# Kernel optimization log

Measured on AMD Instinct MI355X. Metric: run time of the kernel, lower is better.

The kernel has to match this reference:

```python
import jax, jax.numpy as jnp
import numpy as np
from jax import lax

B, CIN, COUT, K, H, W = 16, 512, 512, 3, 64, 64
STYLE_DIM, BASIS, DIRS = 512, 8, 8


def setup_inputs() -> dict:
    key = jax.random.key(0)
    ks = jax.random.split(key, 8)
    return {
        "x": jax.random.normal(ks[0], (B, CIN, H, W), jnp.float32),
        "style": jax.random.normal(ks[1], (B, STYLE_DIM), jnp.float32),
        "weight": jax.random.normal(ks[2], (1, COUT, CIN, K, K), jnp.float32),
        "mod_w": jax.random.normal(ks[3], (CIN, STYLE_DIM), jnp.float32) * 0.02,
        "mod_b": jnp.ones((CIN,), jnp.float32),
        "basis_vectors": jax.random.normal(ks[4], (BASIS, 1, COUT, CIN, K, K), jnp.float32),
        "shifts_coords": jax.random.normal(ks[5], (DIRS, BASIS), jnp.float32),
        "batch_shifts": jax.random.uniform(ks[6], (B,), jnp.float32),
        "batch_directions": jax.random.randint(ks[7], (B,), 0, DIRS),
    }


def reference(x, style, weight, mod_w, mod_b, basis_vectors, shifts_coords,
              batch_shifts, batch_directions):
    batch, in_ch, h, w = x.shape
    out_ch, k = weight.shape[1], weight.shape[3]
    scale = 1.0 / np.sqrt(in_ch * k * k)  # StyleGAN2 equalized-lr scale

    # --- deformation: per-sample weight delta from basis subspace ---
    coefs = shifts_coords[batch_directions]                     # [B, basis]
    bv = basis_vectors.reshape(basis_vectors.shape[0], -1)      # [basis, O*I*k*k]
    delta = coefs @ bv                                          # [B, P]
    nrm = jnp.linalg.norm(delta, axis=1, keepdims=True)
    delta = delta / jnp.maximum(nrm, 1e-12) * batch_shifts[:, None]
    delta = delta.reshape(batch, out_ch, in_ch, k, k)
    wgt = weight + delta                                        # [B, O, I, k, k]

    # --- style modulation + demodulation ---
    s = style @ mod_w.T + mod_b                                 # [B, I]
    wgt = scale * wgt * s[:, None, :, None, None]
    demod = lax.rsqrt(jnp.sum(wgt * wgt, axis=(2, 3, 4)) + 1e-8)  # [B, O]
    wgt = wgt * demod[:, :, None, None, None]

    # --- grouped conv, groups = batch ---
    wgt = wgt.reshape(batch * out_ch, in_ch, k, k)
    xg = x.reshape(1, batch * in_ch, h, w)
    pad = k // 2
    out = lax.conv_general_dilated(
        xg, wgt, window_strides=(1, 1), padding=[(pad, pad), (pad, pad)],
        feature_group_count=batch,
        dimension_numbers=("NCHW", "OIHW", "NCHW"))
    return out.reshape(batch, out_ch, h, w)
```

## Files before the change

kernel.cpp:

```cpp
#include <hip/hip_runtime.h>


typedef __attribute__((ext_vector_type(8))) short bf16x8;
typedef __attribute__((ext_vector_type(4))) float f32x4;

__device__ __forceinline__ unsigned short f2bf(float f) {
  unsigned u = __float_as_uint(f);
  return (unsigned short)((u + 0x7FFFu + ((u >> 16) & 1u)) >> 16);
}

__device__ __forceinline__ void gl_lds16(const void* g, void* l) {
  __builtin_amdgcn_global_load_lds(
      (const __attribute__((address_space(1))) void*)g,
      (__attribute__((address_space(3))) void*)l, 16, 0, 0);
}

template <int N> __device__ __forceinline__ void vm_wait() {
  if constexpr (N == 4) asm volatile("s_waitcnt vmcnt(4)" ::: "memory");
  else if constexpr (N == 0) asm volatile("s_waitcnt vmcnt(0)" ::: "memory");
}

__global__ __launch_bounds__(256) void k_pad(const float* __restrict__ x,
                                             unsigned short* __restrict__ xp) {
  const int bx = blockIdx.x;
  const int b   = bx >> 9;
  const int rem = bx & 511;
  const int y   = rem >> 3;
  const int cb  = rem & 7;
  const int t = threadIdx.x;
  __shared__ float tile[64][65];
  const float* src = x + ((size_t)(b * 512 + cb * 64) * 4096) + y * 64;
#pragma unroll
  for (int r = 0; r < 4; ++r) {
    int idx = r * 256 + t;
    int ch = idx >> 4;
    int xq = (idx & 15) << 2;
    float4 v = *(const float4*)(src + (size_t)ch * 4096 + xq);
    tile[ch][xq + 0] = v.x; tile[ch][xq + 1] = v.y;
    tile[ch][xq + 2] = v.z; tile[ch][xq + 3] = v.w;
  }
  const uint4 z4 = {0u, 0u, 0u, 0u};
  if (t < 16) {
    const int side = t >> 3;
    const int lo = (t & 7) * 8;
    unsigned short* p =
        xp + (((size_t)(b * 66 + y + 1) * 66 + side * 65) * 512 + cb * 64 + lo);
    *(uint4*)p = z4;
  }
  if (y == 0 || y == 63) {
    const int row = (y == 0) ? 0 : 65;
    for (int idx = t; idx < 528; idx += 256) {
      const int c = idx >> 3;
      const int lo = (idx & 7) * 8;
      unsigned short* p =
          xp + (((size_t)(b * 66 + row) * 66 + c) * 512 + cb * 64 + lo);
      *(uint4*)p = z4;
    }
  }
  __syncthreads();
  const int col = t >> 2;
  const int q = t & 3;
  union { unsigned short u16[16]; uint4 v[2]; } pk;
#pragma unroll
  for (int j = 0; j < 16; ++j) pk.u16[j] = f2bf(tile[q * 16 + j][col]);
  unsigned short* dst =
      xp + (((size_t)(b * 66 + y + 1) * 66 + col + 1) * 512 + cb * 64 + q * 16);
  *(uint4*)dst = pk.v[0];
  *(uint4*)(dst + 8) = pk.v[1];
}

__global__ __launch_bounds__(256) void k_mod(const float* __restrict__ style,
                                             const float* __restrict__ mod_w,
                                             const float* __restrict__ mod_b,
                                             float* __restrict__ smod) {
  const int b = blockIdx.x;
  __shared__ float st[512];
  for (int d = threadIdx.x; d < 512; d += 256) st[d] = style[b * 512 + d];
  __syncthreads();
  for (int i = threadIdx.x; i < 512; i += 256) {
    const float* wr = mod_w + (size_t)i * 512;
    float acc = 0.f;
#pragma unroll 4
    for (int d = 0; d < 512; d += 4) {
      float4 wv = *(const float4*)(wr + d);
      acc += wv.x * st[d] + wv.y * st[d + 1] + wv.z * st[d + 2] + wv.w * st[d + 3];
    }
    smod[b * 512 + i] = acc + mod_b[i];
  }
}

__global__ __launch_bounds__(256, 3) void k_gram(const float* __restrict__ bv,
                                                 float* __restrict__ G) {
  const int P4 = 589824;
  float a[36];
#pragma unroll
  for (int c = 0; c < 36; ++c) a[c] = 0.f;
  const float4* bv4 = (const float4*)bv;
  for (int p = blockIdx.x * 256 + threadIdx.x; p < P4; p += gridDim.x * 256) {
    float4 v[8];
#pragma unroll
    for (int k = 0; k < 8; ++k) v[k] = bv4[(size_t)k * P4 + p];
    int c = 0;
#pragma unroll
    for (int i = 0; i < 8; ++i)
#pragma unroll
      for (int j = i; j < 8; ++j) {
        a[c] += v[i].x * v[j].x + v[i].y * v[j].y + v[i].z * v[j].z +
                v[i].w * v[j].w;
        ++c;
      }
  }
#pragma unroll
  for (int c = 0; c < 36; ++c)
#pragma unroll
    for (int off = 32; off > 0; off >>= 1) a[c] += __shfl_down(a[c], off);
  __shared__ float red[4][36];
  const int wv = threadIdx.x >> 6;
  if ((threadIdx.x & 63) == 0)
#pragma unroll
    for (int c = 0; c < 36; ++c) red[wv][c] = a[c];
  __syncthreads();
  if (threadIdx.x < 36)
    atomicAdd(&G[threadIdx.x], red[0][threadIdx.x] + red[1][threadIdx.x] +
                                   red[2][threadIdx.x] + red[3][threadIdx.x]);
}

__global__ void k_amp(const float* __restrict__ shifts_coords,
                      const float* __restrict__ batch_shifts,
                      const int* __restrict__ dirs, const float* __restrict__ G,
                      float* __restrict__ camp) {
  const int b = threadIdx.x;
  if (b < 16) {
    const int dir = dirs[b];
    float c[8];
    for (int k = 0; k < 8; ++k) c[k] = shifts_coords[dir * 8 + k];
    float n2 = 0.f;
    int idx = 0;
    for (int i = 0; i < 8; ++i)
      for (int j = i; j < 8; ++j) {
        float g = G[idx++];
        n2 += (i == j) ? c[i] * c[i] * g : 2.f * c[i] * c[j] * g;
      }
    float nrm = sqrtf(fmaxf(n2, 0.f));
    float amp = batch_shifts[b] / fmaxf(nrm, 1e-12f);
    for (int k = 0; k < 8; ++k) camp[b * 8 + k] = c[k] * amp;
  }
}

__global__ __launch_bounds__(512) void k_weights(const float* __restrict__ weight,
                                                 const float* __restrict__ bv,
                                                 const float* __restrict__ smod,
                                                 const float* __restrict__ camp,
                                                 unsigned short* __restrict__ wgt,
                                                 float* __restrict__ demod) {
  const int o = blockIdx.x;
  const int i = threadIdx.x;
  __shared__ float cl[128];
  __shared__ float red[8][16];
  if (threadIdx.x < 128) cl[threadIdx.x] = camp[threadIdx.x];
  __syncthreads();
  const float scl = 0.014731391274719738f;
  float sm[16];
#pragma unroll
  for (int b = 0; b < 16; ++b) sm[b] = smod[b * 512 + i] * scl;
  float ssq[16];
#pragma unroll
  for (int b = 0; b < 16; ++b) ssq[b] = 0.f;
  const size_t base = ((size_t)o * 512 + i) * 9;
#pragma unroll
  for (int g = 0; g < 3; ++g) {
    float w[3], v[8][3];
#pragma unroll
    for (int q = 0; q < 3; ++q) w[q] = weight[base + g * 3 + q];
#pragma unroll
    for (int k = 0; k < 8; ++k)
#pragma unroll
      for (int q = 0; q < 3; ++q)
        v[k][q] = bv[(size_t)k * 2359296 + base + g * 3 + q];
#pragma unroll
    for (int b = 0; b < 16; ++b) {
#pragma unroll
      for (int q = 0; q < 3; ++q) {
        float d = w[q];
#pragma unroll
        for (int k = 0; k < 8; ++k) d = fmaf(cl[b * 8 + k], v[k][q], d);
        float wv = d * sm[b];
        ssq[b] = fmaf(wv, wv, ssq[b]);
        wgt[(((size_t)(b * 9 + g * 3 + q) * 512 + o) << 9) + i] = f2bf(wv);
      }
    }
  }
#pragma unroll
  for (int b = 0; b < 16; ++b)
#pragma unroll
    for (int off = 32; off > 0; off >>= 1) ssq[b] += __shfl_down(ssq[b], off);
  const int wv_ = threadIdx.x >> 6;
  if ((threadIdx.x & 63) == 0)
#pragma unroll
    for (int b = 0; b < 16; ++b) red[wv_][b] = ssq[b];
  __syncthreads();
  if (threadIdx.x < 16) {
    float s = 0.f;
#pragma unroll
    for (int wq = 0; wq < 8; ++wq) s += red[wq][threadIdx.x];
    demod[threadIdx.x * 512 + o] = rsqrtf(s + 1e-8f);
  }
}

__global__ __launch_bounds__(512, 1) void k_conv(
    const unsigned short* __restrict__ xp, const unsigned short* __restrict__ wgt,
    const float* __restrict__ demod, float* __restrict__ out) {
  extern __shared__ unsigned char smem[];
  const int tid = threadIdx.x;
  const int l = tid & 63;
  const int w = tid >> 6;
  const int wo = w >> 2;
  const int wn = w & 3;

  const int bid = blockIdx.x;
  const int bz = (bid & 7) * 64 + (bid >> 3);
  const int b = bz >> 5;
  const int tt = bz & 31;
  const int o0 = (tt >> 4) << 8;
  const int tn = tt & 15;
  const int n0 = tn << 8;
  const int y0 = tn << 2;

  size_t aOff[2], pBase[2];
  int sOff[2];
#pragma unroll
  for (int r = 0; r < 2; ++r) {
    const int idx = r * 512 + tid;
    const int row = idx >> 2;
    const int slot = idx & 3;
    aOff[r] = ((size_t)(o0 + row) << 10) + slot * 16;
    pBase[r] = (size_t)(b * 66 + y0 + (row >> 6)) * 66 + (row & 63);
    sOff[r] = slot * 16;
  }

  const char* wgtc = (const char*)wgt;
  const char* xpc = (const char*)xp;

  auto stage = [&](unsigned char* buf, int kt) {
    const int kk = kt >> 4;
    const int is = kt & 15;
    const int ky = kk / 3;
    const int kx = kk - ky * 3;
    const size_t aPlane = ((size_t)(b * 9 + kk) << 19) + ((size_t)is << 6);
    unsigned char* lA = buf;
    unsigned char* lB = buf + 16384;
#pragma unroll
    for (int r = 0; r < 2; ++r)
      gl_lds16(wgtc + aPlane + aOff[r], lA + (r * 512 + tid) * 16);
#pragma unroll
    for (int r = 0; r < 2; ++r)
      gl_lds16(xpc + (((pBase[r] + ky * 66 + kx) << 10) + ((size_t)is << 6) +
                      sOff[r]),
               lB + (r * 512 + tid) * 16);
  };

  f32x4 acc[8][4];
  const f32x4 zz = {0.f, 0.f, 0.f, 0.f};
#pragma unroll
  for (int mi = 0; mi < 8; ++mi)
#pragma unroll
    for (int ni = 0; ni < 4; ++ni) acc[mi][ni] = zz;
  bf16x8 af[8], bf[4];

  const int rdoff = (l >> 4) << 4;

  unsigned char* p0 = smem;
  unsigned char* p1 = smem + 32768;
  unsigned char* p2 = smem + 65536;
  stage(p0, 0);
  stage(p1, 1);
  vm_wait<4>();
  __builtin_amdgcn_s_barrier();
  __builtin_amdgcn_sched_barrier(0);

#pragma unroll 1
  for (int kt = 0; kt < 144; ++kt) {
    const unsigned char* lA = p0;
    const unsigned char* lB = p0 + 16384;
#pragma unroll
    for (int ni = 0; ni < 4; ++ni) {
      const int row = wn * 64 + ni * 16 + (l & 15);
      bf[ni] = *(const bf16x8*)(lB + row * 64 + rdoff);
    }
#pragma unroll
    for (int mi = 0; mi < 8; ++mi) {
      const int row = wo * 128 + mi * 16 + (l & 15);
      af[mi] = *(const bf16x8*)(lA + row * 64 + rdoff);
    }
    if (kt <= 141) stage(p2, kt + 2);
    __builtin_amdgcn_s_setprio(1);
#pragma unroll
    for (int mi = 0; mi < 8; ++mi)
#pragma unroll
      for (int ni = 0; ni < 4; ++ni)
        acc[mi][ni] = __builtin_amdgcn_mfma_f32_16x16x32_bf16(
            af[mi], bf[ni], acc[mi][ni], 0, 0, 0);
    __builtin_amdgcn_s_setprio(0);
    __builtin_amdgcn_sched_barrier(0);
    if (kt <= 141) vm_wait<4>();
    else if (kt == 142) vm_wait<0>();
    if (kt <= 142) {
      __builtin_amdgcn_s_barrier();
      __builtin_amdgcn_sched_barrier(0);
    }
    unsigned char* tmp = p0; p0 = p1; p1 = p2; p2 = tmp;
  }

  float* outb = out + (size_t)(b * 512 + o0) * 4096 + n0;
#pragma unroll
  for (int mi = 0; mi < 8; ++mi) {
    const int orow = wo * 128 + mi * 16 + ((l >> 4) << 2);
    float dm[4];
#pragma unroll
    for (int r = 0; r < 4; ++r) dm[r] = demod[b * 512 + o0 + orow + r];
#pragma unroll
    for (int ni = 0; ni < 4; ++ni) {
      const int pix = wn * 64 + ni * 16 + (l & 15);
#pragma unroll
      for (int r = 0; r < 4; ++r)
        outb[(size_t)(orow + r) * 4096 + pix] = acc[mi][ni][r] * dm[r];
    }
  }
}

extern "C" void kernel_launch(void* const* d_in, const int* in_sizes, int n_in,
                              void* d_out, int out_size, void* d_ws,
                              size_t ws_size, hipStream_t stream) {
  const float* x      = (const float*)d_in[0];
  const float* style  = (const float*)d_in[1];
  const float* weight = (const float*)d_in[2];
  const float* mod_w  = (const float*)d_in[3];
  const float* mod_b  = (const float*)d_in[4];
  const float* bv     = (const float*)d_in[5];
  const float* sc     = (const float*)d_in[6];
  const float* bsh    = (const float*)d_in[7];
  const int*   bdir   = (const int*)d_in[8];
  float* out = (float*)d_out;

  char* ws = (char*)d_ws;
  unsigned short* xp  = (unsigned short*)(ws);
  unsigned short* wgt = (unsigned short*)(ws + 71368704);
  float* G     = (float*)(ws + 146866176);
  float* camp  = (float*)(ws + 146866432);
  float* smod  = (float*)(ws + 146866944);
  float* demod = (float*)(ws + 146899712);

  hipFuncSetAttribute((const void*)k_conv,
                      hipFuncAttributeMaxDynamicSharedMemorySize, 98304);

  hipMemsetAsync(G, 0, 256, stream);
  k_pad<<<8192, 256, 0, stream>>>(x, xp);
  k_mod<<<16, 256, 0, stream>>>(style, mod_w, mod_b, smod);
  k_gram<<<1024, 256, 0, stream>>>(bv, G);
  k_amp<<<1, 64, 0, stream>>>(sc, bsh, bdir, G, camp);
  k_weights<<<512, 512, 0, stream>>>(weight, bv, smod, camp, wgt, demod);
  k_conv<<<512, 512, 98304, stream>>>(xp, wgt, demod, out);
}
```

Baseline: 437.0 us.

## Shrink conv tile to 256x128, swizzle LDS, and raise occupancy

The implicit-GEMM conv tile shrinks from 256x256 to 256 output channels by 128 pixels, which doubles the grid to 1024 blocks and cuts accumulators per wave from 32 to 16 MFMA tiles. LDS per block drops to 72KB, and launch bounds now allow more than one block per CU. An XOR swizzle is added to the LDS layout for both A and B to avoid bank conflicts on the fragment reads. Addressing switches to 32-bit offsets. The trade-off is less data reuse per tile (more global and L2 traffic for weights) in exchange for better occupancy and latency hiding.

After: 452.5 us. 1.04x slower.

```diff
diff --git a/kernel.cpp b/kernel.cpp
--- a/kernel.cpp
+++ b/kernel.cpp
@@ -16,7 +16,7 @@
 }
 
 template <int N> __device__ __forceinline__ void vm_wait() {
-  if constexpr (N == 4) asm volatile("s_waitcnt vmcnt(4)" ::: "memory");
+  if constexpr (N == 3) asm volatile("s_waitcnt vmcnt(3)" ::: "memory");
   else if constexpr (N == 0) asm volatile("s_waitcnt vmcnt(0)" ::: "memory");
 }
 
@@ -207,38 +207,42 @@
   }
 }
 
-__global__ __launch_bounds__(512, 1) void k_conv(
+__global__ __launch_bounds__(512, 4) void k_conv(
     const unsigned short* __restrict__ xp, const unsigned short* __restrict__ wgt,
     const float* __restrict__ demod, float* __restrict__ out) {
   extern __shared__ unsigned char smem[];
   const int tid = threadIdx.x;
   const int l = tid & 63;
   const int w = tid >> 6;
-  const int wo = w >> 2;
-  const int wn = w & 3;
+  const int wr = w >> 1;
+  const int wc = w & 1;
 
   const int bid = blockIdx.x;
-  const int bz = (bid & 7) * 64 + (bid >> 3);
-  const int b = bz >> 5;
-  const int tt = bz & 31;
-  const int o0 = (tt >> 4) << 8;
-  const int tn = tt & 15;
-  const int n0 = tn << 8;
-  const int y0 = tn << 2;
-
-  size_t aOff[2], pBase[2];
-  int sOff[2];
+  const int bz = (bid & 7) * 128 + (bid >> 3);
+  const int b = bz >> 6;
+  const int tt = bz & 63;
+  const int o0 = (tt >> 5) << 8;
+  const int tn = tt & 31;
+  const int n0 = tn << 7;
+  const int y0 = tn << 1;
+
+  unsigned aOff[2];
 #pragma unroll
   for (int r = 0; r < 2; ++r) {
     const int idx = r * 512 + tid;
     const int row = idx >> 2;
-    const int slot = idx & 3;
-    aOff[r] = ((size_t)(o0 + row) << 10) + slot * 16;
-    pBase[r] = (size_t)(b * 66 + y0 + (row >> 6)) * 66 + (row & 63);
-    sOff[r] = slot * 16;
-  }
-
-  const char* wgtc = (const char*)wgt;
+    const int sc_ = (idx & 3) ^ ((row >> 1) & 3);
+    aOff[r] = ((unsigned)(o0 + row) << 10) + sc_ * 16;
+  }
+  unsigned bOff;
+  {
+    const int row = tid >> 2;
+    const int sc_ = (tid & 3) ^ ((row >> 1) & 3);
+    bOff = ((unsigned)((b * 66 + y0 + (row >> 6)) * 66 + (row & 63)) << 10) +
+           sc_ * 16;
+  }
+
+  const char* wgtB = (const char*)wgt + ((size_t)(b * 9) << 19);
   const char* xpc = (const char*)xp;
 
   auto stage = [&](unsigned char* buf, int kt) {
@@ -246,35 +250,31 @@
     const int is = kt & 15;
     const int ky = kk / 3;
     const int kx = kk - ky * 3;
-    const size_t aPlane = ((size_t)(b * 9 + kk) << 19) + ((size_t)is << 6);
-    unsigned char* lA = buf;
-    unsigned char* lB = buf + 16384;
+    const unsigned aPl = ((unsigned)kk << 19) + ((unsigned)is << 6);
+    const unsigned bPl = ((unsigned)(ky * 66 + kx) << 10) + ((unsigned)is << 6);
 #pragma unroll
     for (int r = 0; r < 2; ++r)
-      gl_lds16(wgtc + aPlane + aOff[r], lA + (r * 512 + tid) * 16);
-#pragma unroll
-    for (int r = 0; r < 2; ++r)
-      gl_lds16(xpc + (((pBase[r] + ky * 66 + kx) << 10) + ((size_t)is << 6) +
-                      sOff[r]),
-               lB + (r * 512 + tid) * 16);
+      gl_lds16(wgtB + aPl + aOff[r], buf + (r * 512 + tid) * 16);
+    gl_lds16(xpc + bPl + bOff, buf + 16384 + tid * 16);
   };
 
-  f32x4 acc[8][4];
+  f32x4 acc[4][4];
   const f32x4 zz = {0.f, 0.f, 0.f, 0.f};
 #pragma unroll
-  for (int mi = 0; mi < 8; ++mi)
+  for (int mi = 0; mi < 4; ++mi)
 #pragma unroll
     for (int ni = 0; ni < 4; ++ni) acc[mi][ni] = zz;
-  bf16x8 af[8], bf[4];
-
-  const int rdoff = (l >> 4) << 4;
+  bf16x8 af[4], bf[4];
+
+  const int lq = l & 15;
+  const int ls = l >> 4;
 
   unsigned char* p0 = smem;
-  unsigned char* p1 = smem + 32768;
-  unsigned char* p2 = smem + 65536;
+  unsigned char* p1 = smem + 24576;
+  unsigned char* p2 = smem + 49152;
   stage(p0, 0);
   stage(p1, 1);
-  vm_wait<4>();
+  vm_wait<3>();
   __builtin_amdgcn_s_barrier();
   __builtin_amdgcn_sched_barrier(0);
 
@@ -284,25 +284,25 @@
     const unsigned char* lB = p0 + 16384;
 #pragma unroll
     for (int ni = 0; ni < 4; ++ni) {
-      const int row = wn * 64 + ni * 16 + (l & 15);
-      bf[ni] = *(const bf16x8*)(lB + row * 64 + rdoff);
-    }
-#pragma unroll
-    for (int mi = 0; mi < 8; ++mi) {
-      const int row = wo * 128 + mi * 16 + (l & 15);
-      af[mi] = *(const bf16x8*)(lA + row * 64 + rdoff);
+      const int row = wc * 64 + ni * 16 + lq;
+      bf[ni] = *(const bf16x8*)(lB + row * 64 + ((ls ^ ((row >> 1) & 3)) << 4));
+    }
+#pragma unroll
+    for (int mi = 0; mi < 4; ++mi) {
+      const int row = wr * 64 + mi * 16 + lq;
+      af[mi] = *(const bf16x8*)(lA + row * 64 + ((ls ^ ((row >> 1) & 3)) << 4));
     }
     if (kt <= 141) stage(p2, kt + 2);
     __builtin_amdgcn_s_setprio(1);
 #pragma unroll
-    for (int mi = 0; mi < 8; ++mi)
+    for (int mi = 0; mi < 4; ++mi)
 #pragma unroll
       for (int ni = 0; ni < 4; ++ni)
         acc[mi][ni] = __builtin_amdgcn_mfma_f32_16x16x32_bf16(
             af[mi], bf[ni], acc[mi][ni], 0, 0, 0);
     __builtin_amdgcn_s_setprio(0);
     __builtin_amdgcn_sched_barrier(0);
-    if (kt <= 141) vm_wait<4>();
+    if (kt <= 141) vm_wait<3>();
     else if (kt == 142) vm_wait<0>();
     if (kt <= 142) {
       __builtin_amdgcn_s_barrier();
@@ -313,14 +313,14 @@
 
   float* outb = out + (size_t)(b * 512 + o0) * 4096 + n0;
 #pragma unroll
-  for (int mi = 0; mi < 8; ++mi) {
-    const int orow = wo * 128 + mi * 16 + ((l >> 4) << 2);
+  for (int mi = 0; mi < 4; ++mi) {
+    const int orow = wr * 64 + mi * 16 + ls * 4;
     float dm[4];
 #pragma unroll
     for (int r = 0; r < 4; ++r) dm[r] = demod[b * 512 + o0 + orow + r];
 #pragma unroll
     for (int ni = 0; ni < 4; ++ni) {
-      const int pix = wn * 64 + ni * 16 + (l & 15);
+      const int pix = wc * 64 + ni * 16 + lq;
 #pragma unroll
       for (int r = 0; r < 4; ++r)
         outb[(size_t)(orow + r) * 4096 + pix] = acc[mi][ni][r] * dm[r];
@@ -351,7 +351,7 @@
   float* demod = (float*)(ws + 146899712);
 
   hipFuncSetAttribute((const void*)k_conv,
-                      hipFuncAttributeMaxDynamicSharedMemorySize, 98304);
+                      hipFuncAttributeMaxDynamicSharedMemorySize, 73728);
 
   hipMemsetAsync(G, 0, 256, stream);
   k_pad<<<8192, 256, 0, stream>>>(x, xp);
@@ -359,5 +359,5 @@
   k_gram<<<1024, 256, 0, stream>>>(bv, G);
   k_amp<<<1, 64, 0, stream>>>(sc, bsh, bdir, G, camp);
   k_weights<<<512, 512, 0, stream>>>(weight, bv, smod, camp, wgt, demod);
-  k_conv<<<512, 512, 98304, stream>>>(xp, wgt, demod, out);
-}
+  k_conv<<<1024, 512, 73728, stream>>>(xp, wgt, demod, out);
+}
```

## Load weight fragments directly to registers and double-buffer activations in LDS

Applied to the files above, without the earlier changes.

The conv kernel no longer stages the weight (A) tile through LDS. Each wave now loads its A fragments straight from global memory into registers, ping-ponging between two register sets. Only the activation (B) tile goes through LDS, with two buffers and an XOR-swizzled layout meant to avoid bank conflicts. This cuts LDS from 96KB to 32KB and raises launch bounds to allow 2 blocks per CU, but it doubles register use for A fragments and waits on vmcnt(0) every step, which may expose global load latency.

Measured after the change: 827.4 us. +89.4%, slower.

```diff
diff --git a/kernel.cpp b/kernel.cpp
--- a/kernel.cpp
+++ b/kernel.cpp
@@ -15,9 +15,8 @@
       (__attribute__((address_space(3))) void*)l, 16, 0, 0);
 }
 
-template <int N> __device__ __forceinline__ void vm_wait() {
-  if constexpr (N == 4) asm volatile("s_waitcnt vmcnt(4)" ::: "memory");
-  else if constexpr (N == 0) asm volatile("s_waitcnt vmcnt(0)" ::: "memory");
+__device__ __forceinline__ void vm_wait0() {
+  asm volatile("s_waitcnt vmcnt(0)" ::: "memory");
 }
 
 __global__ __launch_bounds__(256) void k_pad(const float* __restrict__ x,
@@ -207,7 +206,7 @@
   }
 }
 
-__global__ __launch_bounds__(512, 1) void k_conv(
+__global__ __launch_bounds__(512, 2) void k_conv(
     const unsigned short* __restrict__ xp, const unsigned short* __restrict__ wgt,
     const float* __restrict__ demod, float* __restrict__ out) {
   extern __shared__ unsigned char smem[];
@@ -216,6 +215,8 @@
   const int w = tid >> 6;
   const int wo = w >> 2;
   const int wn = w & 3;
+  const int lq = l & 15;
+  const int ls = l >> 4;
 
   const int bid = blockIdx.x;
   const int bz = (bid & 7) * 64 + (bid >> 3);
@@ -226,38 +227,30 @@
   const int n0 = tn << 8;
   const int y0 = tn << 2;
 
-  size_t aOff[2], pBase[2];
-  int sOff[2];
+  const char* wgtA = (const char*)wgt + ((size_t)(b * 9) << 19) +
+                     ((size_t)o0 << 10);
+  unsigned a_voff[8];
+#pragma unroll
+  for (int mi = 0; mi < 8; ++mi)
+    a_voff[mi] = ((unsigned)(wo * 128 + mi * 16 + lq) << 10) + (ls << 4);
+
+  unsigned bSrc[2];
 #pragma unroll
   for (int r = 0; r < 2; ++r) {
     const int idx = r * 512 + tid;
     const int row = idx >> 2;
-    const int slot = idx & 3;
-    aOff[r] = ((size_t)(o0 + row) << 10) + slot * 16;
-    pBase[r] = (size_t)(b * 66 + y0 + (row >> 6)) * 66 + (row & 63);
-    sOff[r] = slot * 16;
-  }
-
-  const char* wgtc = (const char*)wgt;
+    const int sl = (idx & 3) ^ ((row >> 1) & 3);
+    bSrc[r] = ((unsigned)((b * 66 + y0 + (row >> 6)) * 66 + (row & 63)) << 10) +
+              sl * 16;
+  }
+  unsigned bRd[4];
+#pragma unroll
+  for (int ni = 0; ni < 4; ++ni) {
+    const int row = wn * 64 + ni * 16 + lq;
+    bRd[ni] = row * 64 + ((ls ^ ((row >> 1) & 3)) << 4);
+  }
+
   const char* xpc = (const char*)xp;
-
-  auto stage = [&](unsigned char* buf, int kt) {
-    const int kk = kt >> 4;
-    const int is = kt & 15;
-    const int ky = kk / 3;
-    const int kx = kk - ky * 3;
-    const size_t aPlane = ((size_t)(b * 9 + kk) << 19) + ((size_t)is << 6);
-    unsigned char* lA = buf;
-    unsigned char* lB = buf + 16384;
-#pragma unroll
-    for (int r = 0; r < 2; ++r)
-      gl_lds16(wgtc + aPlane + aOff[r], lA + (r * 512 + tid) * 16);
-#pragma unroll
-    for (int r = 0; r < 2; ++r)
-      gl_lds16(xpc + (((pBase[r] + ky * 66 + kx) << 10) + ((size_t)is << 6) +
-                      sOff[r]),
-               lB + (r * 512 + tid) * 16);
-  };
 
   f32x4 acc[8][4];
   const f32x4 zz = {0.f, 0.f, 0.f, 0.f};
@@ -265,62 +258,72 @@
   for (int mi = 0; mi < 8; ++mi)
 #pragma unroll
     for (int ni = 0; ni < 4; ++ni) acc[mi][ni] = zz;
-  bf16x8 af[8], bf[4];
-
-  const int rdoff = (l >> 4) << 4;
-
-  unsigned char* p0 = smem;
-  unsigned char* p1 = smem + 32768;
-  unsigned char* p2 = smem + 65536;
-  stage(p0, 0);
-  stage(p1, 1);
-  vm_wait<4>();
+  bf16x8 afA[8], afB[8], bf[4];
+
+  {
+#pragma unroll
+    for (int r = 0; r < 2; ++r)
+      gl_lds16(xpc + bSrc[r], smem + (r * 512 + tid) * 16);
+#pragma unroll
+    for (int mi = 0; mi < 8; ++mi)
+      afA[mi] = *(const bf16x8*)(wgtA + a_voff[mi]);
+  }
+  vm_wait0();
   __builtin_amdgcn_s_barrier();
   __builtin_amdgcn_sched_barrier(0);
 
-#pragma unroll 1
-  for (int kt = 0; kt < 144; ++kt) {
-    const unsigned char* lA = p0;
-    const unsigned char* lB = p0 + 16384;
-#pragma unroll
-    for (int ni = 0; ni < 4; ++ni) {
-      const int row = wn * 64 + ni * 16 + (l & 15);
-      bf[ni] = *(const bf16x8*)(lB + row * 64 + rdoff);
-    }
-#pragma unroll
-    for (int mi = 0; mi < 8; ++mi) {
-      const int row = wo * 128 + mi * 16 + (l & 15);
-      af[mi] = *(const bf16x8*)(lA + row * 64 + rdoff);
-    }
-    if (kt <= 141) stage(p2, kt + 2);
+  auto body = [&](int s, bf16x8 (&afC)[8], bf16x8 (&afN)[8], int par) {
+    const unsigned char* lB = smem + (par ? 16384 : 0);
+    unsigned char* wB = smem + (par ? 0 : 16384);
+#pragma unroll
+    for (int ni = 0; ni < 4; ++ni)
+      bf[ni] = *(const bf16x8*)(lB + bRd[ni]);
+    if (s < 143) {
+      const int s1 = s + 1;
+      const int kk1 = s1 >> 4;
+      const int is1 = s1 & 15;
+      const char* aT = wgtA + ((size_t)kk1 << 19) + ((unsigned)is1 << 6);
+#pragma unroll
+      for (int mi = 0; mi < 8; ++mi)
+        afN[mi] = *(const bf16x8*)(aT + a_voff[mi]);
+      const int ky1 = kk1 / 3;
+      const int kx1 = kk1 - ky1 * 3;
+      const unsigned tOff =
+          ((unsigned)(ky1 * 66 + kx1) << 10) + ((unsigned)is1 << 6);
+#pragma unroll
+      for (int r = 0; r < 2; ++r)
+        gl_lds16(xpc + bSrc[r] + tOff, wB + (r * 512 + tid) * 16);
+    }
     __builtin_amdgcn_s_setprio(1);
 #pragma unroll
     for (int mi = 0; mi < 8; ++mi)
 #pragma unroll
       for (int ni = 0; ni < 4; ++ni)
         acc[mi][ni] = __builtin_amdgcn_mfma_f32_16x16x32_bf16(
-            af[mi], bf[ni], acc[mi][ni], 0, 0, 0);
+            afC[mi], bf[ni], acc[mi][ni], 0, 0, 0);
     __builtin_amdgcn_s_setprio(0);
     __builtin_amdgcn_sched_barrier(0);
-    if (kt <= 141) vm_wait<4>();
-    else if (kt == 142) vm_wait<0>();
-    if (kt <= 142) {
-      __builtin_amdgcn_s_barrier();
-      __builtin_amdgcn_sched_barrier(0);
-    }
-    unsigned char* tmp = p0; p0 = p1; p1 = p2; p2 = tmp;
+    vm_wait0();
+    __builtin_amdgcn_s_barrier();
+    __builtin_amdgcn_sched_barrier(0);
+  };
+
+#pragma unroll 1
+  for (int s = 0; s < 144; s += 2) {
+    body(s, afA, afB, 0);
+    body(s + 1, afB, afA, 1);
   }
 
   float* outb = out + (size_t)(b * 512 + o0) * 4096 + n0;
 #pragma unroll
   for (int mi = 0; mi < 8; ++mi) {
-    const int orow = wo * 128 + mi * 16 + ((l >> 4) << 2);
+    const int orow = wo * 128 + mi * 16 + ls * 4;
     float dm[4];
 #pragma unroll
     for (int r = 0; r < 4; ++r) dm[r] = demod[b * 512 + o0 + orow + r];
 #pragma unroll
     for (int ni = 0; ni < 4; ++ni) {
-      const int pix = wn * 64 + ni * 16 + (l & 15);
+      const int pix = wn * 64 + ni * 16 + lq;
 #pragma unroll
       for (int r = 0; r < 4; ++r)
         outb[(size_t)(orow + r) * 4096 + pix] = acc[mi][ni][r] * dm[r];
@@ -351,7 +354,7 @@
   float* demod = (float*)(ws + 146899712);
 
   hipFuncSetAttribute((const void*)k_conv,
-                      hipFuncAttributeMaxDynamicSharedMemorySize, 98304);
+                      hipFuncAttributeMaxDynamicSharedMemorySize, 32768);
 
   hipMemsetAsync(G, 0, 256, stream);
   k_pad<<<8192, 256, 0, stream>>>(x, xp);
@@ -359,5 +362,5 @@
   k_gram<<<1024, 256, 0, stream>>>(bv, G);
   k_amp<<<1, 64, 0, stream>>>(sc, bsh, bdir, G, camp);
   k_weights<<<512, 512, 0, stream>>>(weight, bv, smod, camp, wgt, demod);
-  k_conv<<<512, 512, 98304, stream>>>(xp, wgt, demod, out);
-}
+  k_conv<<<512, 512, 32768, stream>>>(xp, wgt, demod, out);
+}
```
